# Performance work log

Measured on AMD Instinct MI355X. Metric: run time of the kernel, lower is better.

Reference implementation:

```python
import jax, jax.numpy as jnp
import numpy as np

N = 50000      # nodes (particles)
E = 1600000    # edges
G = 2000       # graphs (jets)
NEG_SLOPE = 0.2

def setup_inputs() -> dict:
    key = jax.random.key(0)
    ks = jax.random.split(key, 18)
    p = lambda k, s: (jax.random.normal(k, s, jnp.float32) * 0.1)
    return {
        'x': jax.random.normal(ks[0], (N, 3), jnp.float32),
        'edge_index': jax.random.randint(ks[1], (2, E), 0, N, dtype=jnp.int64),
        'batch': jnp.sort(jax.random.randint(ks[2], (N,), 0, G, dtype=jnp.int64)),
        'W1': p(ks[3], (3, 128)),  'a1s': p(ks[4], (4, 32)),  'a1d': p(ks[5], (4, 32)),  'b1': p(ks[6], (128,)),
        'W2': p(ks[7], (128, 128)),'a2s': p(ks[8], (4, 32)),  'a2d': p(ks[9], (4, 32)),  'b2': p(ks[10], (128,)),
        'W3': p(ks[11], (128, 32)),'a3s': p(ks[12], (1, 32)), 'a3d': p(ks[13], (1, 32)), 'b3': p(ks[14], (32,)),
        'Wh': p(ks[15], (32, 2)),  'bh': p(ks[16], (2,)),
    }

def gat_conv(x, src, dst, W, a_src, a_dst, b, concat):
    """PyG GATConv (eval mode): gather-score-softmax-scatter over edges (src->dst)."""
    n = x.shape[0]
    H, C = a_src.shape
    h = (x @ W).reshape(n, H, C)                         # [N,H,C]
    es = jnp.sum(h * a_src, axis=-1)                     # [N,H] source scores
    ed = jnp.sum(h * a_dst, axis=-1)                     # [N,H] dest scores
    e = jax.nn.leaky_relu(es[src] + ed[dst], NEG_SLOPE)  # [E,H]
    # neighbor-wise (per destination node) stable softmax
    m = jax.ops.segment_max(e, dst, num_segments=n)      # [N,H]
    m = jax.lax.stop_gradient(jnp.where(jnp.isfinite(m), m, 0.0))
    w = jnp.exp(e - m[dst])
    z = jax.ops.segment_sum(w, dst, num_segments=n)      # [N,H]
    alpha = w / (z[dst] + 1e-16)                         # [E,H]
    out = jax.ops.segment_sum(h[src] * alpha[:, :, None], dst, num_segments=n)  # [N,H,C]
    out = out.reshape(n, H * C) if concat else out.mean(axis=1)
    return out + b

def reference(x, edge_index, batch, W1, a1s, a1d, b1, W2, a2s, a2d, b2,
              W3, a3s, a3d, b3, Wh, bh):
    n = x.shape[0]
    loops = jnp.arange(n, dtype=edge_index.dtype)        # add_self_loops=True
    src = jnp.concatenate([edge_index[0], loops])
    dst = jnp.concatenate([edge_index[1], loops])
    h = jax.nn.elu(gat_conv(x, src, dst, W1, a1s, a1d, b1, True))
    h = jax.nn.elu(gat_conv(h, src, dst, W2, a2s, a2d, b2, True))
    h = jax.nn.elu(gat_conv(h, src, dst, W3, a3s, a3d, b3, False))
    cnt = jax.ops.segment_sum(jnp.ones((n,), h.dtype), batch, num_segments=G)
    pooled = jax.ops.segment_sum(h, batch, num_segments=G) / jnp.maximum(cnt, 1.0)[:, None]
    return pooled @ Wh + bh                              # [G, n_classes]
```

## Files before the change

kernel.cpp:

```cpp
#include <hip/hip_runtime.h>

#define CAP 80
#define NXCD 8
#define SUBW 128
#define NSUBR 49
#define SQC 96
#define QCAPB 512
#define CHUNK 2048

typedef int vint4 __attribute__((ext_vector_type(4)));
__device__ __forceinline__ vint4 ntload_i4(const int* p){ return __builtin_nontemporal_load((const vint4*)p); }

__device__ __forceinline__ float lrelu02(float x){ return x > 0.f ? x : 0.2f*x; }
__device__ __forceinline__ float eluf(float x){ return x > 0.f ? x : (__expf(x)-1.f); }
__device__ __forceinline__ unsigned short f2bf(float x){
  unsigned u = __float_as_uint(x);
  u += 0x7fffu + ((u >> 16) & 1u);
  return (unsigned short)(u >> 16);
}
__device__ __forceinline__ float bf2f(unsigned short b){
  return __uint_as_float(((unsigned)b) << 16);
}

__global__ void cnt_kernel(const int* __restrict__ batch, float* __restrict__ cnt, int n){
  int i = blockIdx.x*blockDim.x + threadIdx.x;
  if (i < n) atomicAdd(&cnt[batch[i]], 1.f);
}

__global__ void radix_proj1_kernel(const int* __restrict__ src, const int* __restrict__ dst,
                                   int E, int n, int nrb, int RW, int qcap,
                                   int* __restrict__ gcur, int2* __restrict__ qbuf,
                                   const float* __restrict__ x, const float* __restrict__ W,
                                   const float* __restrict__ as_, const float* __restrict__ ad_,
                                   unsigned short* __restrict__ hout, float* __restrict__ es,
                                   float* __restrict__ ed){
  if ((int)blockIdx.x < nrb){
    __shared__ int2 q[NXCD][QCAPB];
    __shared__ int qc[NXCD];
    __shared__ int qbase[NXCD];
    int t = threadIdx.x;
    if (t < NXCD) qc[t] = 0;
    __syncthreads();
    int e0 = blockIdx.x*CHUNK + t*8;
    if (e0 + 8 <= E){
      vint4 d40 = ntload_i4(dst + e0), d41 = ntload_i4(dst + e0 + 4);
      vint4 s40 = ntload_i4(src + e0), s41 = ntload_i4(src + e0 + 4);
      int dd[8] = {d40[0],d40[1],d40[2],d40[3],d41[0],d41[1],d41[2],d41[3]};
      int ss[8] = {s40[0],s40[1],s40[2],s40[3],s41[0],s41[1],s41[2],s41[3]};
      #pragma unroll
      for (int k = 0; k < 8; ++k){
        int qi = min(dd[k] / RW, NXCD-1);
        int pos = atomicAdd(&qc[qi], 1);
        if (pos < QCAPB) q[qi][pos] = make_int2(ss[k], dd[k]);
      }
    } else {
      for (int e = e0; e < E; ++e){
        int d = dst[e];
        int qi = min(d / RW, NXCD-1);
        int pos = atomicAdd(&qc[qi], 1);
        if (pos < QCAPB) q[qi][pos] = make_int2(src[e], d);
      }
    }
    __syncthreads();
    if (t < NXCD) qbase[t] = atomicAdd(&gcur[t], min(qc[t], QCAPB));
    __syncthreads();
    #pragma unroll
    for (int qi = 0; qi < NXCD; ++qi){
      int cq = min(qc[qi], QCAPB);
      int2* gq = qbuf + (size_t)qi*qcap;
      int b0 = qbase[qi];
      for (int i = t; i < cq; i += 256)
        if (b0 + i < qcap) gq[b0 + i] = q[qi][i];
    }
  } else {
    __shared__ float xs[2][3];
    int node0 = ((int)blockIdx.x - nrb) * 2;
    int t = threadIdx.x;
    if (t < 6){
      int nn = node0 + t/3;
      xs[t/3][t%3] = (nn < n) ? x[(size_t)nn*3 + t%3] : 0.f;
    }
    __syncthreads();
    int node = node0 + t / 128;
    int o = t % 128;
    if (node >= n) return;
    const float* xr = xs[t / 128];
    float acc = 0.f;
    #pragma unroll
    for (int k = 0; k < 3; ++k) acc = fmaf(xr[k], W[k*128 + o], acc);
    hout[(size_t)node*128 + o] = f2bf(acc);
    float ts = acc * as_[o];
    float td = acc * ad_[o];
    #pragma unroll
    for (int m = 16; m >= 1; m >>= 1){
      ts += __shfl_xor(ts, m);
      td += __shfl_xor(td, m);
    }
    if ((o & 31) == 0){
      es[node*4 + (o>>5)] = ts;
      ed[node*4 + (o>>5)] = td;
    }
  }
}

__global__ void radix_sub_kernel(const int2* __restrict__ qbuf, const int* __restrict__ gcur,
                                 int qcap, int bpr, int scap,
                                 int* __restrict__ scnt, int2* __restrict__ sbuf){
  __shared__ int2 q[NSUBR][SQC];
  __shared__ int qc[NSUBR];
  __shared__ int qb[NSUBR];
  int r  = blockIdx.x / bpr;
  int bi = blockIdx.x % bpr;
  int t = threadIdx.x;
  if (t < NSUBR) qc[t] = 0;
  __syncthreads();
  int len = min(gcur[r], qcap);
  int i0 = bi*CHUNK + t*8;
  const int2* qg = qbuf + (size_t)r*qcap;
  #pragma unroll
  for (int k = 0; k < 8; ++k){
    int i = i0 + k;
    if (i < len){
      int2 e = qg[i];
      int qi = (e.y >> 7) - r*NSUBR;
      int pos = atomicAdd(&qc[qi], 1);
      if (pos < SQC) q[qi][pos] = e;
    }
  }
  __syncthreads();
  if (t < NSUBR){
    int c = min(qc[t], SQC);
    qb[t] = c ? atomicAdd(&scnt[r*NSUBR + t], c) : 0;
  }
  __syncthreads();
  for (int qi = 0; qi < NSUBR; ++qi){
    int cq = min(qc[qi], SQC);
    if (!cq) continue;
    int2* gq = sbuf + (size_t)(r*NSUBR + qi)*scap;
    int b0 = qb[qi];
    for (int i = t; i < cq; i += 256)
      if (b0 + i < scap) gq[b0 + i] = q[qi][i];
  }
}

__global__ void bucket_csr_kernel(const int2* __restrict__ sbuf, const int* __restrict__ scnt,
                                  int scap, unsigned short* __restrict__ col,
                                  int* __restrict__ deg, int n){
  __shared__ unsigned short colS[SUBW*CAP];
  __shared__ int cur[SUBW];
  int sb = blockIdx.x;
  int t = threadIdx.x;
  {
    uint4 zz = make_uint4(0,0,0,0);
    uint4* cz = (uint4*)colS;
    for (int i = t; i < SUBW*CAP*2/16; i += 256) cz[i] = zz;
  }
  if (t < SUBW) cur[t] = 0;
  __syncthreads();
  int len = min(scnt[sb], scap);
  const int2* sq = sbuf + (size_t)sb*scap;
  for (int i = t; i < len; i += 256){
    int2 e = sq[i];
    int r = e.y & (SUBW-1);
    int slot = atomicAdd(&cur[r], 1);
    if (slot < CAP) colS[r*CAP + slot] = (unsigned short)e.x;
  }
  __syncthreads();
  int base = sb*SUBW;
  int nb = min(SUBW, n - base);
  const uint4* srcp = (const uint4*)colS;
  uint4* dstp = (uint4*)(col + (size_t)base*CAP);
  for (int i = t; i < nb*10; i += 256) dstp[i] = srcp[i];
  if (t < nb) deg[base + t] = min(cur[t], CAP);
}

template<int OUT, int NPT, int H>
__global__ void proj_tiled_kernel(const float* __restrict__ x, const float* __restrict__ W,
                                  const float* __restrict__ as_, const float* __restrict__ ad_,
                                  unsigned short* __restrict__ hout, float* __restrict__ es,
                                  float* __restrict__ ed, int n){
  constexpr int OG = OUT / 4;
  constexpr int NG = 256 / OG;
  constexpr int NODES = NG * NPT;
  __shared__ float xs[128][NODES + 1];
  int node0 = blockIdx.x * NODES;
  int t = threadIdx.x;
  for (int i = t; i < NODES*32; i += 256){
    int nl = i >> 5, kc = i & 31;
    int nn = node0 + nl;
    float4 v = make_float4(0.f,0.f,0.f,0.f);
    if (nn < n) v = *(const float4*)(x + (size_t)nn*128 + kc*4);
    xs[kc*4+0][nl] = v.x;
    xs[kc*4+1][nl] = v.y;
    xs[kc*4+2][nl] = v.z;
    xs[kc*4+3][nl] = v.w;
  }
  __syncthreads();
  int og = t % OG;
  int ng = t / OG;
  float acc[NPT][4];
  #pragma unroll
  for (int p = 0; p < NPT; ++p){ acc[p][0]=0.f; acc[p][1]=0.f; acc[p][2]=0.f; acc[p][3]=0.f; }
  const float* wp = W + og*4;
  #pragma unroll 4
  for (int k = 0; k < 128; ++k){
    float4 w = *(const float4*)(wp + (size_t)k*OUT);
    #pragma unroll
    for (int p = 0; p < NPT; ++p){
      float xv = xs[k][ng*NPT + p];
      acc[p][0] = fmaf(xv, w.x, acc[p][0]);
      acc[p][1] = fmaf(xv, w.y, acc[p][1]);
      acc[p][2] = fmaf(xv, w.z, acc[p][2]);
      acc[p][3] = fmaf(xv, w.w, acc[p][3]);
    }
  }
  int o = og*4;
  float as0 = as_[o], as1 = as_[o+1], as2 = as_[o+2], as3 = as_[o+3];
  float ad0 = ad_[o], ad1 = ad_[o+1], ad2 = ad_[o+2], ad3 = ad_[o+3];
  #pragma unroll
  for (int p = 0; p < NPT; ++p){
    int node = node0 + ng*NPT + p;
    float ts = acc[p][0]*as0 + acc[p][1]*as1 + acc[p][2]*as2 + acc[p][3]*as3;
    float td = acc[p][0]*ad0 + acc[p][1]*ad1 + acc[p][2]*ad2 + acc[p][3]*ad3;
    #pragma unroll
    for (int m = 4; m >= 1; m >>= 1){
      ts += __shfl_xor(ts, m);
      td += __shfl_xor(td, m);
    }
    if (node < n){
      ushort4 hb;
      hb.x = f2bf(acc[p][0]); hb.y = f2bf(acc[p][1]);
      hb.z = f2bf(acc[p][2]); hb.w = f2bf(acc[p][3]);
      *(ushort4*)(hout + (size_t)node*OUT + o) = hb;
      if ((og & 7) == 0){
        int head = og >> 3;
        es[node*H + head] = ts;
        ed[node*H + head] = td;
      }
    }
  }
}

__global__ void agg128_kernel(const unsigned short* __restrict__ h, const float* __restrict__ es,
                              const float* __restrict__ ed, const int* __restrict__ deg,
                              const unsigned short* __restrict__ col, const float* __restrict__ bias,
                              float* __restrict__ out, int n){
  __shared__ float wsS[4][4][CAP];
  int wv = threadIdx.x >> 6;
  int node = blockIdx.x*4 + wv;
  int lane = threadIdx.x & 63;
  if (node >= n) return;
  int beg = node*CAP;
  int degN = min(deg[node], CAP);
  int degR = (degN + 15) & ~15;
  int eh = lane >> 2, hh = lane & 3;
  float edh = ed[node*4 + hh];
  float zp = 0.f;
  for (int base = 0; base < degR; base += 16){
    int e = base + eh;
    float w = 0.f;
    if (e < degN){
      int s = (int)col[beg + e];
      w = __expf(lrelu02(es[s*4 + hh] + edh));
    }
    wsS[wv][hh][e] = w;
    zp += w;
  }
  #pragma unroll
  for (int m = 4; m <= 32; m <<= 1) zp += __shfl_xor(zp, m);
  int head = lane >> 4;
  float z = __shfl(zp, head);
  float ed_h = __shfl(edh, head);
  float a0 = 0.f, a1 = 0.f;
  const unsigned short* colp = col + beg;
  for (int base = 0; base < degR; base += 16){
    uint4 c0 = *(const uint4*)(colp + base);
    uint4 c1 = *(const uint4*)(colp + base + 8);
    unsigned cw[8] = {c0.x,c0.y,c0.z,c0.w,c1.x,c1.y,c1.z,c1.w};
    int s[16];
    #pragma unroll
    for (int k = 0; k < 8; ++k){ s[2*k] = cw[k] & 0xffffu; s[2*k+1] = cw[k] >> 16; }
    float4 w0 = *(const float4*)&wsS[wv][head][base];
    float4 w1 = *(const float4*)&wsS[wv][head][base+4];
    float4 w2 = *(const float4*)&wsS[wv][head][base+8];
    float4 w3 = *(const float4*)&wsS[wv][head][base+12];
    float wk[16] = {w0.x,w0.y,w0.z,w0.w, w1.x,w1.y,w1.z,w1.w,
                    w2.x,w2.y,w2.z,w2.w, w3.x,w3.y,w3.z,w3.w};
    unsigned u[16];
    #pragma unroll
    for (int k = 0; k < 16; ++k) u[k] = *(const unsigned*)(h + (size_t)s[k]*128 + 2*lane);
    #pragma unroll
    for (int k = 0; k < 16; ++k){
      a0 = fmaf(wk[k], __uint_as_float(u[k] << 16), a0);
      a1 = fmaf(wk[k], __uint_as_float(u[k] & 0xffff0000u), a1);
    }
  }
  {
    float w = __expf(lrelu02(es[node*4 + head] + ed_h));
    unsigned u = *(const unsigned*)(h + (size_t)node*128 + 2*lane);
    z += w;
    a0 = fmaf(w, __uint_as_float(u << 16), a0);
    a1 = fmaf(w, __uint_as_float(u & 0xffff0000u), a1);
  }
  float inv = 1.f / (z + 1e-16f);
  int o = 2*lane;
  float2 r;
  r.x = eluf(a0*inv + bias[o]);
  r.y = eluf(a1*inv + bias[o+1]);
  *(float2*)(out + (size_t)node*128 + o) = r;
}

__global__ void agg32_pool_kernel(const unsigned short* __restrict__ h, const float* __restrict__ es,
                                  const float* __restrict__ ed, const int* __restrict__ deg,
                                  const unsigned short* __restrict__ col, const float* __restrict__ bias,
                                  const int* __restrict__ batch, float* __restrict__ pooled, int n){
  __shared__ float wsS[4][CAP];
  int wv = threadIdx.x >> 6;
  int node = blockIdx.x*4 + wv;
  int lane = threadIdx.x & 63;
  if (node >= n) return;
  int beg = node*CAP;
  int degN = min(deg[node], CAP);
  int degR = (degN + 15) & ~15;
  float ed0 = ed[node];
  float zp = 0.f;
  for (int base = 0; base < CAP; base += 64){
    int e = base + lane;
    float w = 0.f;
    if (e < degN){
      int s = (int)col[beg + e];
      w = __expf(lrelu02(es[s] + ed0));
    }
    if (e < CAP) wsS[wv][e] = w;
    zp += w;
  }
  #pragma unroll
  for (int m = 1; m < 64; m <<= 1) zp += __shfl_xor(zp, m);
  float z = zp;
  int half = lane >> 5;
  int c = lane & 31;
  float a0 = 0.f;
  const unsigned short* colp = col + beg;
  for (int base = 0; base < degR; base += 16){
    int b = base + 8*half;
    uint4 c4 = *(const uint4*)(colp + b);
    unsigned cw[4] = {c4.x,c4.y,c4.z,c4.w};
    int s[8];
    #pragma unroll
    for (int k = 0; k < 4; ++k){ s[2*k] = cw[k] & 0xffffu; s[2*k+1] = cw[k] >> 16; }
    float4 w01 = *(const float4*)&wsS[wv][b];
    float4 w23 = *(const float4*)&wsS[wv][b+4];
    float wk[8] = {w01.x,w01.y,w01.z,w01.w, w23.x,w23.y,w23.z,w23.w};
    float hv[8];
    #pragma unroll
    for (int k = 0; k < 8; ++k) hv[k] = bf2f(h[(size_t)s[k]*32 + c]);
    #pragma unroll
    for (int k = 0; k < 8; ++k) a0 = fmaf(wk[k], hv[k], a0);
  }
  a0 += __shfl_xor(a0, 32);
  {
    float w = __expf(lrelu02(es[node] + ed0));
    float hv = bf2f(h[(size_t)node*32 + c]);
    z += w;
    a0 = fmaf(w, hv, a0);
  }
  if (half == 0){
    float inv = 1.f / (z + 1e-16f);
    float val = eluf(a0*inv + bias[c]);
    int g = batch[node];
    atomicAdd(&pooled[g*32 + c], val);
  }
}

__global__ void head_kernel(const float* __restrict__ pooled, const float* __restrict__ cnt,
                            const float* __restrict__ Wh, const float* __restrict__ bh,
                            float* __restrict__ out, int G){
  int g = blockIdx.x*blockDim.x + threadIdx.x;
  if (g >= G) return;
  float inv = 1.f / fmaxf(cnt[g], 1.f);
  float o0 = bh[0], o1 = bh[1];
  #pragma unroll
  for (int c = 0; c < 32; ++c){
    float p = pooled[g*32 + c] * inv;
    o0 = fmaf(p, Wh[c*2+0], o0);
    o1 = fmaf(p, Wh[c*2+1], o1);
  }
  out[g*2+0] = o0;
  out[g*2+1] = o1;
}

extern "C" void kernel_launch(void* const* d_in, const int* in_sizes, int n_in,
                              void* d_out, int out_size, void* d_ws, size_t ws_size,
                              hipStream_t stream){
  const float* x   = (const float*)d_in[0];
  const int*   ei  = (const int*)d_in[1];
  const int* batch = (const int*)d_in[2];
  const float* W1  = (const float*)d_in[3];
  const float* a1s = (const float*)d_in[4];
  const float* a1d = (const float*)d_in[5];
  const float* b1  = (const float*)d_in[6];
  const float* W2  = (const float*)d_in[7];
  const float* a2s = (const float*)d_in[8];
  const float* a2d = (const float*)d_in[9];
  const float* b2  = (const float*)d_in[10];
  const float* W3  = (const float*)d_in[11];
  const float* a3s = (const float*)d_in[12];
  const float* a3d = (const float*)d_in[13];
  const float* b3  = (const float*)d_in[14];
  const float* Wh  = (const float*)d_in[15];
  const float* bh  = (const float*)d_in[16];
  const int n = in_sizes[0] / 3;
  const int E = in_sizes[1] / 2;
  const int G = out_size / 2;
  float* out = (float*)d_out;

  const int RW   = NSUBR * SUBW;
  const int NSB  = (n + SUBW - 1) / SUBW;
  const int qcap = E/NXCD * 5/4 + 4096;
  const int scap = (int)((long long)E*SUBW/n * 5/4) + 512;

  char* p = (char*)d_ws;
  auto alloc = [&](size_t bytes)->char*{ char* r = p; p += (bytes + 255) & ~(size_t)255; return r; };
  float* buf_x            = (float*)alloc((size_t)n*128*4);
  unsigned short* buf_h   = (unsigned short*)alloc((size_t)n*128*2);
  float* es     = (float*)alloc((size_t)n*4*4);
  float* ed     = (float*)alloc((size_t)n*4*4);
  float* pooled = (float*)alloc((size_t)G*33*4);
  float* cnt    = pooled + (size_t)G*32;
  int* deg      = (int*)alloc((size_t)n*4);
  unsigned short* col = (unsigned short*)alloc((size_t)n*CAP*2);
  int* gcur     = (int*)alloc(NXCD*4);
  int* scnt     = (int*)alloc((size_t)(NXCD*NSUBR)*4);
  int2* qbuf    = (int2*)alloc((size_t)NXCD*qcap*8);
  int2* sbuf    = (int2*)alloc((size_t)NXCD*NSUBR*scap*8);

  const int* srcr = ei;
  const int* dstr = ei + E;

  hipMemsetAsync(gcur, 0, NXCD*4, stream);
  hipMemsetAsync(scnt, 0, (size_t)(NXCD*NSUBR)*4, stream);
  hipMemsetAsync(pooled, 0, (size_t)G*33*4, stream);

  cnt_kernel<<<(n+255)/256, 256, 0, stream>>>(batch, cnt, n);

  int nrb = (E + CHUNK - 1) / CHUNK;
  int proj_blocks = (n + 1) / 2;
  radix_proj1_kernel<<<nrb + proj_blocks, 256, 0, stream>>>(
      srcr, dstr, E, n, nrb, RW, qcap, gcur, qbuf, x, W1, a1s, a1d, buf_h, es, ed);
  int bpr = (qcap + CHUNK - 1) / CHUNK;
  radix_sub_kernel<<<NXCD*bpr, 256, 0, stream>>>(qbuf, gcur, qcap, bpr, scap, scnt, sbuf);
  bucket_csr_kernel<<<NSB, 256, 0, stream>>>(sbuf, scnt, scap, col, deg, n);

  agg128_kernel<<<(n+3)/4, 256, 0, stream>>>(buf_h, es, ed, deg, col, b1, buf_x, n);
  proj_tiled_kernel<128,4,4><<<(n+31)/32, 256, 0, stream>>>(buf_x, W2, a2s, a2d, buf_h, es, ed, n);
  agg128_kernel<<<(n+3)/4, 256, 0, stream>>>(buf_h, es, ed, deg, col, b2, buf_x, n);
  proj_tiled_kernel<32,2,1><<<(n+63)/64, 256, 0, stream>>>(buf_x, W3, a3s, a3d, buf_h, es, ed, n);
  agg32_pool_kernel<<<(n+3)/4, 256, 0, stream>>>(buf_h, es, ed, deg, col, b3, batch, pooled, n);

  head_kernel<<<(G+255)/256, 256, 0, stream>>>(pooled, cnt, Wh, bh, out, G);
}
```

Measured before the change: 293.2 us.

## Pack radix edge entries into 32 bits and store layer activations as bf16

Radix-partition queue entries go from int2 (src,dst) to one 32-bit word holding src in the low 16 bits and the dst offset within its range in the high 16 bits. This halves queue and sub-bucket traffic and the shared-memory staging. The inter-layer activation buffer written by agg128 and read by proj_tiled becomes bf16 instead of fp32, which halves that round trip but adds rounding error. The two counter memsets are merged into one.

```diff
diff --git a/kernel.cpp b/kernel.cpp
--- a/kernel.cpp
+++ b/kernel.cpp
@@ -29,13 +29,13 @@
 
 __global__ void radix_proj1_kernel(const int* __restrict__ src, const int* __restrict__ dst,
                                    int E, int n, int nrb, int RW, int qcap,
-                                   int* __restrict__ gcur, int2* __restrict__ qbuf,
+                                   int* __restrict__ gcur, unsigned* __restrict__ qbuf,
                                    const float* __restrict__ x, const float* __restrict__ W,
                                    const float* __restrict__ as_, const float* __restrict__ ad_,
                                    unsigned short* __restrict__ hout, float* __restrict__ es,
                                    float* __restrict__ ed){
   if ((int)blockIdx.x < nrb){
-    __shared__ int2 q[NXCD][QCAPB];
+    __shared__ unsigned q[NXCD][QCAPB];
     __shared__ int qc[NXCD];
     __shared__ int qbase[NXCD];
     int t = threadIdx.x;
@@ -51,14 +51,14 @@
       for (int k = 0; k < 8; ++k){
         int qi = min(dd[k] / RW, NXCD-1);
         int pos = atomicAdd(&qc[qi], 1);
-        if (pos < QCAPB) q[qi][pos] = make_int2(ss[k], dd[k]);
+        if (pos < QCAPB) q[qi][pos] = ((unsigned)(dd[k] - qi*RW) << 16) | (unsigned)ss[k];
       }
     } else {
       for (int e = e0; e < E; ++e){
         int d = dst[e];
         int qi = min(d / RW, NXCD-1);
         int pos = atomicAdd(&qc[qi], 1);
-        if (pos < QCAPB) q[qi][pos] = make_int2(src[e], d);
+        if (pos < QCAPB) q[qi][pos] = ((unsigned)(d - qi*RW) << 16) | (unsigned)src[e];
       }
     }
     __syncthreads();
@@ -67,7 +67,7 @@
     #pragma unroll
     for (int qi = 0; qi < NXCD; ++qi){
       int cq = min(qc[qi], QCAPB);
-      int2* gq = qbuf + (size_t)qi*qcap;
+      unsigned* gq = qbuf + (size_t)qi*qcap;
       int b0 = qbase[qi];
       for (int i = t; i < cq; i += 256)
         if (b0 + i < qcap) gq[b0 + i] = q[qi][i];
@@ -103,10 +103,10 @@
   }
 }
 
-__global__ void radix_sub_kernel(const int2* __restrict__ qbuf, const int* __restrict__ gcur,
+__global__ void radix_sub_kernel(const unsigned* __restrict__ qbuf, const int* __restrict__ gcur,
                                  int qcap, int bpr, int scap,
-                                 int* __restrict__ scnt, int2* __restrict__ sbuf){
-  __shared__ int2 q[NSUBR][SQC];
+                                 int* __restrict__ scnt, unsigned* __restrict__ sbuf){
+  __shared__ unsigned q[NSUBR][SQC];
   __shared__ int qc[NSUBR];
   __shared__ int qb[NSUBR];
   int r  = blockIdx.x / bpr;
@@ -116,13 +116,13 @@
   __syncthreads();
   int len = min(gcur[r], qcap);
   int i0 = bi*CHUNK + t*8;
-  const int2* qg = qbuf + (size_t)r*qcap;
+  const unsigned* qg = qbuf + (size_t)r*qcap;
   #pragma unroll
   for (int k = 0; k < 8; ++k){
     int i = i0 + k;
     if (i < len){
-      int2 e = qg[i];
-      int qi = (e.y >> 7) - r*NSUBR;
+      unsigned e = qg[i];
+      int qi = (int)(e >> 23);
       int pos = atomicAdd(&qc[qi], 1);
       if (pos < SQC) q[qi][pos] = e;
     }
@@ -136,14 +136,14 @@
   for (int qi = 0; qi < NSUBR; ++qi){
     int cq = min(qc[qi], SQC);
     if (!cq) continue;
-    int2* gq = sbuf + (size_t)(r*NSUBR + qi)*scap;
+    unsigned* gq = sbuf + (size_t)(r*NSUBR + qi)*scap;
     int b0 = qb[qi];
     for (int i = t; i < cq; i += 256)
       if (b0 + i < scap) gq[b0 + i] = q[qi][i];
   }
 }
 
-__global__ void bucket_csr_kernel(const int2* __restrict__ sbuf, const int* __restrict__ scnt,
+__global__ void bucket_csr_kernel(const unsigned* __restrict__ sbuf, const int* __restrict__ scnt,
                                   int scap, unsigned short* __restrict__ col,
                                   int* __restrict__ deg, int n){
   __shared__ unsigned short colS[SUBW*CAP];
@@ -158,12 +158,12 @@
   if (t < SUBW) cur[t] = 0;
   __syncthreads();
   int len = min(scnt[sb], scap);
-  const int2* sq = sbuf + (size_t)sb*scap;
+  const unsigned* sq = sbuf + (size_t)sb*scap;
   for (int i = t; i < len; i += 256){
-    int2 e = sq[i];
-    int r = e.y & (SUBW-1);
+    unsigned e = sq[i];
+    int r = (int)((e >> 16) & (SUBW-1));
     int slot = atomicAdd(&cur[r], 1);
-    if (slot < CAP) colS[r*CAP + slot] = (unsigned short)e.x;
+    if (slot < CAP) colS[r*CAP + slot] = (unsigned short)(e & 0xffffu);
   }
   __syncthreads();
   int base = sb*SUBW;
@@ -175,7 +175,7 @@
 }
 
 template<int OUT, int NPT, int H>
-__global__ void proj_tiled_kernel(const float* __restrict__ x, const float* __restrict__ W,
+__global__ void proj_tiled_kernel(const unsigned short* __restrict__ xb, const float* __restrict__ W,
                                   const float* __restrict__ as_, const float* __restrict__ ad_,
                                   unsigned short* __restrict__ hout, float* __restrict__ es,
                                   float* __restrict__ ed, int n){
@@ -185,15 +185,13 @@
   __shared__ float xs[128][NODES + 1];
   int node0 = blockIdx.x * NODES;
   int t = threadIdx.x;
-  for (int i = t; i < NODES*32; i += 256){
-    int nl = i >> 5, kc = i & 31;
+  for (int i = t; i < NODES*64; i += 256){
+    int nl = i >> 6, ku = i & 63;
     int nn = node0 + nl;
-    float4 v = make_float4(0.f,0.f,0.f,0.f);
-    if (nn < n) v = *(const float4*)(x + (size_t)nn*128 + kc*4);
-    xs[kc*4+0][nl] = v.x;
-    xs[kc*4+1][nl] = v.y;
-    xs[kc*4+2][nl] = v.z;
-    xs[kc*4+3][nl] = v.w;
+    unsigned v = 0;
+    if (nn < n) v = ((const unsigned*)(xb + (size_t)nn*128))[ku];
+    xs[2*ku + 0][nl] = __uint_as_float(v << 16);
+    xs[2*ku + 1][nl] = __uint_as_float(v & 0xffff0000u);
   }
   __syncthreads();
   int og = t % OG;
@@ -244,7 +242,7 @@
 __global__ void agg128_kernel(const unsigned short* __restrict__ h, const float* __restrict__ es,
                               const float* __restrict__ ed, const int* __restrict__ deg,
                               const unsigned short* __restrict__ col, const float* __restrict__ bias,
-                              float* __restrict__ out, int n){
+                              unsigned short* __restrict__ outb, int n){
   __shared__ float wsS[4][4][CAP];
   int wv = threadIdx.x >> 6;
   int node = blockIdx.x*4 + wv;
@@ -304,10 +302,9 @@
   }
   float inv = 1.f / (z + 1e-16f);
   int o = 2*lane;
-  float2 r;
-  r.x = eluf(a0*inv + bias[o]);
-  r.y = eluf(a1*inv + bias[o+1]);
-  *(float2*)(out + (size_t)node*128 + o) = r;
+  unsigned r0 = (unsigned)f2bf(eluf(a0*inv + bias[o]));
+  unsigned r1 = (unsigned)f2bf(eluf(a1*inv + bias[o+1]));
+  *(unsigned*)(outb + (size_t)node*128 + o) = (r1 << 16) | r0;
 }
 
 __global__ void agg32_pool_kernel(const unsigned short* __restrict__ h, const float* __restrict__ es,
@@ -421,7 +418,7 @@
 
   char* p = (char*)d_ws;
   auto alloc = [&](size_t bytes)->char*{ char* r = p; p += (bytes + 255) & ~(size_t)255; return r; };
-  float* buf_x            = (float*)alloc((size_t)n*128*4);
+  unsigned short* buf_x   = (unsigned short*)alloc((size_t)n*128*2);
   unsigned short* buf_h   = (unsigned short*)alloc((size_t)n*128*2);
   float* es     = (float*)alloc((size_t)n*4*4);
   float* ed     = (float*)alloc((size_t)n*4*4);
@@ -429,16 +426,16 @@
   float* cnt    = pooled + (size_t)G*32;
   int* deg      = (int*)alloc((size_t)n*4);
   unsigned short* col = (unsigned short*)alloc((size_t)n*CAP*2);
-  int* gcur     = (int*)alloc(NXCD*4);
-  int* scnt     = (int*)alloc((size_t)(NXCD*NSUBR)*4);
-  int2* qbuf    = (int2*)alloc((size_t)NXCD*qcap*8);
-  int2* sbuf    = (int2*)alloc((size_t)NXCD*NSUBR*scap*8);
+  int* ctrs     = (int*)alloc((size_t)(NXCD + NXCD*NSUBR)*4);
+  int* gcur     = ctrs;
+  int* scnt     = ctrs + NXCD;
+  unsigned* qbuf = (unsigned*)alloc((size_t)NXCD*qcap*4);
+  unsigned* sbuf = (unsigned*)alloc((size_t)NXCD*NSUBR*scap*4);
 
   const int* srcr = ei;
   const int* dstr = ei + E;
 
-  hipMemsetAsync(gcur, 0, NXCD*4, stream);
-  hipMemsetAsync(scnt, 0, (size_t)(NXCD*NSUBR)*4, stream);
+  hipMemsetAsync(ctrs, 0, (size_t)(NXCD + NXCD*NSUBR)*4, stream);
   hipMemsetAsync(pooled, 0, (size_t)G*33*4, stream);
 
   cnt_kernel<<<(n+255)/256, 256, 0, stream>>>(batch, cnt, n);
```

After: 283.4 us. 1.03x faster.
